# Optimization experiments

Hardware: AMD Instinct MI355X
Metric: run time of the kernel (lower is better)

## Reference

```python
import jax, jax.numpy as jnp
import numpy as np

B, T, D = 2, 2048, 1024
H = 16
HD = D // H  # 64


def setup_inputs() -> dict:
    key = jax.random.key(0)
    k1, k2, k3, k4, k5 = jax.random.split(key, 5)
    s = 0.02
    return {
        "x": jax.random.normal(k1, (B, T, D), dtype=jnp.float32),
        "Wqkv": jax.random.normal(k2, (D, 3 * D), dtype=jnp.float32) * s,
        "bqkv": jax.random.normal(k3, (3 * D,), dtype=jnp.float32) * s,
        "Wout": jax.random.normal(k4, (D, D), dtype=jnp.float32) * s,
        "bout": jax.random.normal(k5, (D,), dtype=jnp.float32) * s,
    }


def reference(x, Wqkv, bqkv, Wout, bout):
    b, t, c = x.shape
    qkv = (x @ Wqkv + bqkv).reshape(b, t, 3, H, HD)
    q = jnp.transpose(qkv[:, :, 0], (0, 2, 1, 3))  # [B,H,T,HD]
    k = jnp.transpose(qkv[:, :, 1], (0, 2, 1, 3))
    v = jnp.transpose(qkv[:, :, 2], (0, 2, 1, 3))
    att = jnp.einsum("bhqd,bhkd->bhqk", q, k) * (HD ** -0.5)
    mask = jnp.tril(jnp.ones((t, t), dtype=bool))  # causal, no past kv
    att = jnp.where(mask, att, -jnp.inf)
    att = jax.nn.softmax(att, axis=-1)
    y = jnp.einsum("bhqk,bhkd->bhqd", att, v)
    y = jnp.transpose(y, (0, 2, 1, 3)).reshape(b, t, c)
    return y @ Wout + bout
```

## Files before the change

kernel.cpp:

```cpp
#include <hip/hip_runtime.h>
#include <hip/hip_bf16.h>
#include <math.h>

#define B_  2
#define T_  2048
#define D_  1024
#define H_  16
#define HD_ 64

typedef __attribute__((ext_vector_type(8))) short short8;
typedef __attribute__((ext_vector_type(4))) float f32x4;

#if __has_builtin(__builtin_amdgcn_exp2f)
#define EXP2F __builtin_amdgcn_exp2f
#else
#define EXP2F exp2f
#endif

__device__ __forceinline__ ushort f2bf(float x) {
    unsigned u = __builtin_bit_cast(unsigned, x);
    return (ushort)((u + 0x7FFFu + ((u >> 16) & 1u)) >> 16);
}

__device__ __forceinline__ unsigned pack_bf2_fast(float a, float b) {
    unsigned ua = __builtin_bit_cast(unsigned, a) + 0x8000u;
    unsigned ub = __builtin_bit_cast(unsigned, b) + 0x8000u;
    return (ua >> 16) | (ub & 0xFFFF0000u);
}

__device__ __forceinline__ void load_lds_16B(const ushort* g, ushort* l) {
    __builtin_amdgcn_global_load_lds(
        (const __attribute__((address_space(1))) unsigned*)g,
        (__attribute__((address_space(3))) unsigned*)l, 16, 0, 0);
}

__global__ __launch_bounds__(256)
void prep_kernel(const float* __restrict__ x, ushort* __restrict__ xb,
                 const float* __restrict__ Wqkv, ushort* __restrict__ Wqkvt,
                 const float* __restrict__ Wout, ushort* __restrict__ Woutt)
{
    __shared__ ushort Ts[64][65];
    const int bid = blockIdx.x;

    if (bid < 512) {
        const int n4 = (B_ * T_ * D_) / 4;
        for (int i = bid * 256 + threadIdx.x; i < n4; i += 512 * 256) {
            float4 v = ((const float4*)x)[i];
            ushort4 o = { f2bf(v.x), f2bf(v.y), f2bf(v.z), f2bf(v.w) };
            ((ushort4*)xb)[i] = o;
        }
        return;
    }

    const float* W; ushort* Wt; int K, M, m0, k0;
    if (bid < 1280) {
        const int t = bid - 512;
        W = Wqkv; Wt = Wqkvt; K = D_; M = 3 * D_;
        m0 = (t % 48) * 64; k0 = (t / 48) * 64;
    } else {
        const int t = bid - 1280;
        W = Wout; Wt = Woutt; K = D_; M = D_;
        m0 = (t % 16) * 64; k0 = (t / 16) * 64;
    }

    const int tr = threadIdx.x >> 4;
    const int tc = threadIdx.x & 15;
    #pragma unroll
    for (int it = 0; it < 4; it++) {
        int k = tr + it * 16;
        float4 v = *(const float4*)&W[(size_t)(k0 + k) * M + m0 + tc * 4];
        Ts[tc * 4 + 0][k] = f2bf(v.x);
        Ts[tc * 4 + 1][k] = f2bf(v.y);
        Ts[tc * 4 + 2][k] = f2bf(v.z);
        Ts[tc * 4 + 3][k] = f2bf(v.w);
    }
    __syncthreads();
    #pragma unroll
    for (int it = 0; it < 2; it++) {
        const int mr  = (threadIdx.x >> 3) + it * 32;
        const int seg = (threadIdx.x & 7) * 8;
        short8 v;
        #pragma unroll
        for (int r = 0; r < 8; r++) v[r] = (short)Ts[mr][seg + r];
        *(short8*)&Wt[(size_t)(m0 + mr) * K + k0 + seg] = v;
    }
}

__global__ __launch_bounds__(256, 4)
void gemm_qkv(const ushort* __restrict__ A, const ushort* __restrict__ Bt,
              const float* __restrict__ bias,
              ushort* __restrict__ Qg, ushort* __restrict__ Kg,
              ushort* __restrict__ Vtg)
{
    const int K = D_;
    __shared__ __align__(16) ushort lds[16384];
    ushort* Asl = lds;
    ushort* Bsl = lds + 8192;

    const int tid = threadIdx.x;
    const int w  = tid >> 6, L = tid & 63;
    const int lt = L & 15, lq = L >> 4;
    const int wr = w >> 1, wc = w & 1;
    const int m0 = blockIdx.x * 128, n0 = blockIdx.y * 128;
    const int rsub = L >> 3;
    const int pgr  = L & 7;

    f32x4 acc[4][4] = {};

    for (int k0 = 0; k0 < K; k0 += 64) {
        __syncthreads();
        #pragma unroll
        for (int j = 0; j < 4; j++) {
            const int row  = (w * 4 + j) * 8 + rsub;
            const int gran = pgr ^ rsub;
            load_lds_16B(A  + (size_t)(n0 + row) * K + k0 + gran * 8,
                         &Asl[row * 64 + pgr * 8]);
            load_lds_16B(Bt + (size_t)(m0 + row) * K + k0 + gran * 8,
                         &Bsl[row * 64 + pgr * 8]);
        }
        __syncthreads();

        #pragma unroll
        for (int ks = 0; ks < 2; ks++) {
            short8 af[4], bf[4];
            #pragma unroll
            for (int i = 0; i < 4; i++) {
                const int ra = wr * 64 + i * 16 + lt;
                af[i] = *(const short8*)&Asl[ra * 64 + (((ks * 4 + lq) ^ (ra & 7)) * 8)];
                const int rb = wc * 64 + i * 16 + lt;
                bf[i] = *(const short8*)&Bsl[rb * 64 + (((ks * 4 + lq) ^ (rb & 7)) * 8)];
            }
            #pragma unroll
            for (int i = 0; i < 4; i++)
                #pragma unroll
                for (int j = 0; j < 4; j++)
                    acc[i][j] = __builtin_amdgcn_mfma_f32_16x16x32_bf16(af[i], bf[j], acc[i][j], 0, 0, 0);
        }
    }

    __syncthreads();
    const int s  = m0 >> 10;
    const int h0 = (m0 & 1023) >> 6;
    const float qs = (s == 0) ? 0.18033688011112042f : 1.0f;

    if (s < 2) {
        #pragma unroll
        for (int j = 0; j < 4; j++) {
            const int m  = wc * 64 + j * 16 + lt;
            const float bv = bias[m0 + m];
            #pragma unroll
            for (int i = 0; i < 4; i++) {
                const int n = wr * 64 + i * 16 + lq * 4;
                #pragma unroll
                for (int r = 0; r < 4; r++)
                    lds[(n + r) * 128 + m] = f2bf((acc[i][j][r] + bv) * qs);
            }
        }
        __syncthreads();
        ushort* dst = (s == 0 ? Qg : Kg);
        #pragma unroll
        for (int it = 0; it < 8; it++) {
            const int g   = tid + it * 256;
            const int row = g >> 4, c = g & 15;
            const int n = n0 + row;
            const int b = n >> 11, t = n & 2047;
            const int h = h0 + (c >> 3), d = (c & 7) * 8;
            short8 v = *(const short8*)&lds[row * 128 + c * 8];
            *(short8*)&dst[((size_t)(b * H_ + h) * T_ + t) * HD_ + d] = v;
        }
    } else {
        #pragma unroll
        for (int j = 0; j < 4; j++) {
            const int m  = wc * 64 + j * 16 + lt;
            const float bv = bias[m0 + m];
            #pragma unroll
            for (int i = 0; i < 4; i++) {
                const int n = wr * 64 + i * 16 + lq * 4;
                uint2 pk = { pack_bf2_fast(acc[i][j][0] + bv, acc[i][j][1] + bv),
                             pack_bf2_fast(acc[i][j][2] + bv, acc[i][j][3] + bv) };
                *(uint2*)&lds[m * 128 + n] = pk;
            }
        }
        __syncthreads();
        const int b = n0 >> 11, t0 = n0 & 2047;
        #pragma unroll
        for (int it = 0; it < 8; it++) {
            const int g   = tid + it * 256;
            const int row = g >> 4, c = g & 15;
            const int h = h0 + (row >> 6), d = row & 63;
            short8 v = *(const short8*)&lds[row * 128 + c * 8];
            *(short8*)&Vtg[((size_t)(b * H_ + h) * HD_ + d) * T_ + t0 + c * 8] = v;
        }
    }
}

__global__ __launch_bounds__(256, 4)
void gemm_out(const ushort* __restrict__ A, const ushort* __restrict__ Bt,
              const float* __restrict__ bias, float* __restrict__ C)
{
    const int K = D_, M = D_;
    __shared__ __align__(16) ushort lds[8192 + 4096];
    ushort* Asl = lds;
    ushort* Bsl = lds + 8192;

    const int tid = threadIdx.x;
    const int w  = tid >> 6, L = tid & 63;
    const int lt = L & 15, lq = L >> 4;
    const int wr = w >> 1, wc = w & 1;
    const int m0 = blockIdx.x * 64, n0 = blockIdx.y * 128;
    const int rsub = L >> 3;
    const int pgr  = L & 7;

    f32x4 acc[2][4] = {};

    for (int k0 = 0; k0 < K; k0 += 64) {
        __syncthreads();
        #pragma unroll
        for (int j = 0; j < 4; j++) {
            const int row  = (w * 4 + j) * 8 + rsub;
            const int gran = pgr ^ rsub;
            load_lds_16B(A + (size_t)(n0 + row) * K + k0 + gran * 8,
                         &Asl[row * 64 + pgr * 8]);
        }
        #pragma unroll
        for (int j = 0; j < 2; j++) {
            const int row  = (w * 2 + j) * 8 + rsub;
            const int gran = pgr ^ rsub;
            load_lds_16B(Bt + (size_t)(m0 + row) * K + k0 + gran * 8,
                         &Bsl[row * 64 + pgr * 8]);
        }
        __syncthreads();

        #pragma unroll
        for (int ks = 0; ks < 2; ks++) {
            short8 wf[2], yf[4];
            #pragma unroll
            for (int j = 0; j < 2; j++) {
                const int rb = wc * 32 + j * 16 + lt;
                wf[j] = *(const short8*)&Bsl[rb * 64 + (((ks * 4 + lq) ^ (rb & 7)) * 8)];
            }
            #pragma unroll
            for (int i = 0; i < 4; i++) {
                const int ra = wr * 64 + i * 16 + lt;
                yf[i] = *(const short8*)&Asl[ra * 64 + (((ks * 4 + lq) ^ (ra & 7)) * 8)];
            }
            #pragma unroll
            for (int j = 0; j < 2; j++)
                #pragma unroll
                for (int i = 0; i < 4; i++)
                    acc[j][i] = __builtin_amdgcn_mfma_f32_16x16x32_bf16(wf[j], yf[i], acc[j][i], 0, 0, 0);
        }
    }

    #pragma unroll
    for (int j = 0; j < 2; j++) {
        const int mbase = m0 + wc * 32 + j * 16 + lq * 4;
        const float4 bv = *(const float4*)&bias[mbase];
        #pragma unroll
        for (int i = 0; i < 4; i++) {
            const int n = n0 + wr * 64 + i * 16 + lt;
            float4 o = { acc[j][i][0] + bv.x, acc[j][i][1] + bv.y,
                         acc[j][i][2] + bv.z, acc[j][i][3] + bv.w };
            *(float4*)&C[(size_t)n * M + mbase] = o;
        }
    }
}

__global__ __launch_bounds__(256, 4)
void attn_mfma(const ushort* __restrict__ Qg, const ushort* __restrict__ Kg,
               const ushort* __restrict__ Vtg, ushort* __restrict__ yb)
{
    const int h = blockIdx.y, b = blockIdx.z;
    const int flip = ((blockIdx.y >> 3) ^ blockIdx.z) & 1;
    const int qb = flip ? blockIdx.x : (31 - blockIdx.x);
    const int tid = threadIdx.x;
    const int w  = tid >> 6, L = tid & 63;
    const int lt = L & 15, lq = L >> 4;

    __shared__ __align__(16) ushort Ks[128 * 64];
    __shared__ __align__(16) ushort Ps[4][640];

    const size_t bh = (size_t)(b * H_ + h);
    const ushort* Qbase  = Qg  + bh * T_ * HD_;
    const ushort* Kbase  = Kg  + bh * T_ * HD_;
    const ushort* Vf     = Vtg + bh * HD_ * T_ + (size_t)lt * T_ + lq * 8;

    const int q_glob = qb * 64 + w * 16 + lt;
    const short8 qf0 = *(const short8*)(Qbase + (size_t)q_glob * HD_ + lq * 8);
    const short8 qf1 = *(const short8*)(Qbase + (size_t)q_glob * HD_ + 32 + lq * 8);

    f32x4 acc_o[4] = {};
    float lsum = 0.f;

    const int krow = tid >> 3, kpg = tid & 7;
    const int nk = (qb + 2) >> 1;

    for (int kb = 0; kb < nk; kb++) {
        __syncthreads();
        #pragma unroll
        for (int rr = 0; rr < 4; rr++) {
            const int row = krow + 32 * rr;
            load_lds_16B(Kbase + (size_t)(kb * 128 + row) * HD_ + (kpg ^ (row & 7)) * 8,
                         &Ks[row * 64 + kpg * 8]);
        }
        __syncthreads();

        const bool last = (kb == nk - 1);
        const int ksN = (!last || (qb & 1)) ? 4 : 2;
        const int mk0 = last ? ((qb & 1) ? 2 : 0) : 4;

        for (int ks = 0; ks < ksN; ks++) {
            const int key0 = kb * 128 + ks * 32;
            const ushort* vp = Vf + key0;
            short8 vf0 = *(const short8*)(vp);
            short8 vf1 = *(const short8*)(vp + 16 * T_);
            short8 vf2 = *(const short8*)(vp + 32 * T_);
            short8 vf3 = *(const short8*)(vp + 48 * T_);

            const int row0 = (2 * ks) * 16 + lt;
            const int row1 = row0 + 16;
            short8 a00 = *(const short8*)&Ks[row0 * 64 + ((lq ^ (row0 & 7)) * 8)];
            short8 a01 = *(const short8*)&Ks[row0 * 64 + (((4 + lq) ^ (row0 & 7)) * 8)];
            short8 a10 = *(const short8*)&Ks[row1 * 64 + ((lq ^ (row1 & 7)) * 8)];
            short8 a11 = *(const short8*)&Ks[row1 * 64 + (((4 + lq) ^ (row1 & 7)) * 8)];
            f32x4 c0 = {}, c1 = {};
            c0 = __builtin_amdgcn_mfma_f32_16x16x32_bf16(a00, qf0, c0, 0, 0, 0);
            c0 = __builtin_amdgcn_mfma_f32_16x16x32_bf16(a01, qf1, c0, 0, 0, 0);
            c1 = __builtin_amdgcn_mfma_f32_16x16x32_bf16(a10, qf0, c1, 0, 0, 0);
            c1 = __builtin_amdgcn_mfma_f32_16x16x32_bf16(a11, qf1, c1, 0, 0, 0);

            float p[8];
            #pragma unroll
            for (int r = 0; r < 4; r++) { p[r] = EXP2F(c0[r]); p[4 + r] = EXP2F(c1[r]); }
            if (ks >= mk0) {
                const int kq = key0 + lq * 4;
                #pragma unroll
                for (int r = 0; r < 4; r++) {
                    if (kq + r > q_glob)      p[r] = 0.f;
                    if (kq + 16 + r > q_glob) p[4 + r] = 0.f;
                }
            }
            lsum += ((p[0] + p[1]) + (p[2] + p[3])) + ((p[4] + p[5]) + (p[6] + p[7]));
            *(uint2*)&Ps[w][lt * 40 + lq * 4] =
                (uint2){ pack_bf2_fast(p[0], p[1]), pack_bf2_fast(p[2], p[3]) };
            *(uint2*)&Ps[w][lt * 40 + 16 + lq * 4] =
                (uint2){ pack_bf2_fast(p[4], p[5]), pack_bf2_fast(p[6], p[7]) };

            short8 pf = *(const short8*)&Ps[w][lt * 40 + lq * 8];

            acc_o[0] = __builtin_amdgcn_mfma_f32_16x16x32_bf16(pf, vf0, acc_o[0], 0, 0, 0);
            acc_o[1] = __builtin_amdgcn_mfma_f32_16x16x32_bf16(pf, vf1, acc_o[1], 0, 0, 0);
            acc_o[2] = __builtin_amdgcn_mfma_f32_16x16x32_bf16(pf, vf2, acc_o[2], 0, 0, 0);
            acc_o[3] = __builtin_amdgcn_mfma_f32_16x16x32_bf16(pf, vf3, acc_o[3], 0, 0, 0);
        }
    }

    lsum += __shfl_xor(lsum, 16, 64);
    lsum += __shfl_xor(lsum, 32, 64);
    const float inv = 1.0f / lsum;

    float linv[4];
    #pragma unroll
    for (int r = 0; r < 4; r++) linv[r] = __shfl(inv, lq * 4 + r, 64);

    ushort* ybase = yb + (size_t)(b * T_ + qb * 64 + w * 16) * D_ + h * HD_;
    #pragma unroll
    for (int r = 0; r < 4; r++)
        #pragma unroll
        for (int dt = 0; dt < 4; dt++)
            ybase[(size_t)(lq * 4 + r) * D_ + dt * 16 + lt] = f2bf(acc_o[dt][r] * linv[r]);
}

extern "C" void kernel_launch(void* const* d_in, const int* in_sizes, int n_in,
                              void* d_out, int out_size, void* d_ws, size_t ws_size,
                              hipStream_t stream)
{
    const float* x    = (const float*)d_in[0];
    const float* Wqkv = (const float*)d_in[1];
    const float* bqkv = (const float*)d_in[2];
    const float* Wout = (const float*)d_in[3];
    const float* bout = (const float*)d_in[4];
    float* out = (float*)d_out;

    char* ws = (char*)d_ws;
    const size_t NT = (size_t)B_ * T_;
    ushort* xb     = (ushort*)ws;
    ushort* Wqkvt  = (ushort*)(ws + NT * D_ * 2);
    ushort* Woutt  = (ushort*)(ws + NT * D_ * 2 + (size_t)3 * D_ * D_ * 2);
    char*   p      = ws + NT * D_ * 2 + (size_t)4 * D_ * D_ * 2;
    const size_t qkv_elems = (size_t)B_ * H_ * T_ * HD_;
    ushort* Qg  = (ushort*)p;
    ushort* Kg  = (ushort*)(p + qkv_elems * 2);
    ushort* Vtg = (ushort*)(p + qkv_elems * 4);
    ushort* yb  = (ushort*)(p + qkv_elems * 6);

    prep_kernel<<<1536, 256, 0, stream>>>(x, xb, Wqkv, Wqkvt, Wout, Woutt);

    gemm_qkv<<<dim3(3 * D_ / 128, NT / 128), 256, 0, stream>>>(
        xb, Wqkvt, bqkv, Qg, Kg, Vtg);

    attn_mfma<<<dim3(32, H_, B_), 256, 0, stream>>>(Qg, Kg, Vtg, yb);

    gemm_out<<<dim3(D_ / 64, NT / 128), 256, 0, stream>>>(
        yb, Woutt, bout, out);
}
```

Baseline: 197.9 us.

## Double-buffer K and V tiles in LDS with 64-key blocks and fp16 PV

The attention kernel now stages both K and transposed V into double-buffered LDS tiles of 64 keys, prefetching the next tile while computing on the current one. Before, K was loaded in 128-key tiles between two barriers and V was read directly from global memory. Causal masking is now handled per diagonal block using each warp's index. V and P are now stored as fp16 rather than bf16, and the PV product uses the f16 MFMA, which gives extra mantissa precision at the cost of a narrower range. The aim is to hide global-load latency and cut uncoalesced V reads, in exchange for more LDS per block, which could lower occupancy.

```diff
diff --git a/kernel.cpp b/kernel.cpp
--- a/kernel.cpp
+++ b/kernel.cpp
@@ -9,6 +9,7 @@
 #define HD_ 64
 
 typedef __attribute__((ext_vector_type(8))) short short8;
+typedef __attribute__((ext_vector_type(8))) _Float16 half8;
 typedef __attribute__((ext_vector_type(4))) float f32x4;
 
 #if __has_builtin(__builtin_amdgcn_exp2f)
@@ -26,6 +27,10 @@
     unsigned ua = __builtin_bit_cast(unsigned, a) + 0x8000u;
     unsigned ub = __builtin_bit_cast(unsigned, b) + 0x8000u;
     return (ua >> 16) | (ub & 0xFFFF0000u);
+}
+
+__device__ __forceinline__ unsigned pack_h2(float a, float b) {
+    return __builtin_bit_cast(unsigned, __builtin_amdgcn_cvt_pkrtz(a, b));
 }
 
 __device__ __forceinline__ void load_lds_16B(const ushort* g, ushort* l) {
@@ -176,8 +181,8 @@
             #pragma unroll
             for (int i = 0; i < 4; i++) {
                 const int n = wr * 64 + i * 16 + lq * 4;
-                uint2 pk = { pack_bf2_fast(acc[i][j][0] + bv, acc[i][j][1] + bv),
-                             pack_bf2_fast(acc[i][j][2] + bv, acc[i][j][3] + bv) };
+                uint2 pk = { pack_h2(acc[i][j][0] + bv, acc[i][j][1] + bv),
+                             pack_h2(acc[i][j][2] + bv, acc[i][j][3] + bv) };
                 *(uint2*)&lds[m * 128 + n] = pk;
             }
         }
@@ -276,53 +281,64 @@
     const int tid = threadIdx.x;
     const int w  = tid >> 6, L = tid & 63;
     const int lt = L & 15, lq = L >> 4;
-
-    __shared__ __align__(16) ushort Ks[128 * 64];
-    __shared__ __align__(16) ushort Ps[4][640];
+    const int kswz = lt & 7;
+
+    __shared__ __align__(16) ushort Ks [2][64 * 64];
+    __shared__ __align__(16) ushort Vts[2][64 * 64];
+    __shared__ __align__(16) ushort Ps [4][640];
 
     const size_t bh = (size_t)(b * H_ + h);
     const ushort* Qbase  = Qg  + bh * T_ * HD_;
     const ushort* Kbase  = Kg  + bh * T_ * HD_;
-    const ushort* Vf     = Vtg + bh * HD_ * T_ + (size_t)lt * T_ + lq * 8;
-
-    const int q_glob = qb * 64 + w * 16 + lt;
+    const ushort* Vtbase = Vtg + bh * HD_ * T_;
+
+    const int q_in   = w * 16 + lt;
+    const int q_glob = qb * 64 + q_in;
     const short8 qf0 = *(const short8*)(Qbase + (size_t)q_glob * HD_ + lq * 8);
     const short8 qf1 = *(const short8*)(Qbase + (size_t)q_glob * HD_ + 32 + lq * 8);
 
     f32x4 acc_o[4] = {};
     float lsum = 0.f;
 
-    const int krow = tid >> 3, kpg = tid & 7;
-    const int nk = (qb + 2) >> 1;
+    const int srow = tid >> 3, spg = tid & 7;
+    const int nk = qb + 1;
+
+    #pragma unroll
+    for (int rr = 0; rr < 2; rr++) {
+        const int r = srow + 32 * rr;
+        load_lds_16B(Kbase + (size_t)r * HD_ + ((spg ^ (r & 7)) * 8),
+                     &Ks[0][r * 64 + spg * 8]);
+        load_lds_16B(Vtbase + (size_t)r * T_ + ((spg ^ (r & 7)) * 8),
+                     &Vts[0][r * 64 + spg * 8]);
+    }
 
     for (int kb = 0; kb < nk; kb++) {
-        __syncthreads();
-        #pragma unroll
-        for (int rr = 0; rr < 4; rr++) {
-            const int row = krow + 32 * rr;
-            load_lds_16B(Kbase + (size_t)(kb * 128 + row) * HD_ + (kpg ^ (row & 7)) * 8,
-                         &Ks[row * 64 + kpg * 8]);
-        }
-        __syncthreads();
-
-        const bool last = (kb == nk - 1);
-        const int ksN = (!last || (qb & 1)) ? 4 : 2;
-        const int mk0 = last ? ((qb & 1) ? 2 : 0) : 4;
+        const int cur = kb & 1;
+        __syncthreads();
+
+        if (kb + 1 < nk) {
+            const int nxt = cur ^ 1;
+            #pragma unroll
+            for (int rr = 0; rr < 2; rr++) {
+                const int r = srow + 32 * rr;
+                load_lds_16B(Kbase + (size_t)((kb + 1) * 64 + r) * HD_ + ((spg ^ (r & 7)) * 8),
+                             &Ks[nxt][r * 64 + spg * 8]);
+                load_lds_16B(Vtbase + (size_t)r * T_ + (kb + 1) * 64 + ((spg ^ (r & 7)) * 8),
+                             &Vts[nxt][r * 64 + spg * 8]);
+            }
+        }
+
+        const bool diag = (kb == nk - 1);
+        const int ksN = diag ? ((w >> 1) + 1) : 2;
+        const int mkc = diag ? (w >> 1) : 2;
 
         for (int ks = 0; ks < ksN; ks++) {
-            const int key0 = kb * 128 + ks * 32;
-            const ushort* vp = Vf + key0;
-            short8 vf0 = *(const short8*)(vp);
-            short8 vf1 = *(const short8*)(vp + 16 * T_);
-            short8 vf2 = *(const short8*)(vp + 32 * T_);
-            short8 vf3 = *(const short8*)(vp + 48 * T_);
-
-            const int row0 = (2 * ks) * 16 + lt;
+            const int row0 = ks * 32 + lt;
             const int row1 = row0 + 16;
-            short8 a00 = *(const short8*)&Ks[row0 * 64 + ((lq ^ (row0 & 7)) * 8)];
-            short8 a01 = *(const short8*)&Ks[row0 * 64 + (((4 + lq) ^ (row0 & 7)) * 8)];
-            short8 a10 = *(const short8*)&Ks[row1 * 64 + ((lq ^ (row1 & 7)) * 8)];
-            short8 a11 = *(const short8*)&Ks[row1 * 64 + (((4 + lq) ^ (row1 & 7)) * 8)];
+            short8 a00 = *(const short8*)&Ks[cur][row0 * 64 + ((lq ^ kswz) * 8)];
+            short8 a01 = *(const short8*)&Ks[cur][row0 * 64 + (((4 + lq) ^ kswz) * 8)];
+            short8 a10 = *(const short8*)&Ks[cur][row1 * 64 + ((lq ^ kswz) * 8)];
+            short8 a11 = *(const short8*)&Ks[cur][row1 * 64 + (((4 + lq) ^ kswz) * 8)];
             f32x4 c0 = {}, c1 = {};
             c0 = __builtin_amdgcn_mfma_f32_16x16x32_bf16(a00, qf0, c0, 0, 0, 0);
             c0 = __builtin_amdgcn_mfma_f32_16x16x32_bf16(a01, qf1, c0, 0, 0, 0);
@@ -332,26 +348,30 @@
             float p[8];
             #pragma unroll
             for (int r = 0; r < 4; r++) { p[r] = EXP2F(c0[r]); p[4 + r] = EXP2F(c1[r]); }
-            if (ks >= mk0) {
-                const int kq = key0 + lq * 4;
+            if (ks == mkc) {
+                const int key0 = ks * 32 + lq * 4;
                 #pragma unroll
                 for (int r = 0; r < 4; r++) {
-                    if (kq + r > q_glob)      p[r] = 0.f;
-                    if (kq + 16 + r > q_glob) p[4 + r] = 0.f;
+                    if (key0 + r > q_in)      p[r] = 0.f;
+                    if (key0 + 16 + r > q_in) p[4 + r] = 0.f;
                 }
             }
             lsum += ((p[0] + p[1]) + (p[2] + p[3])) + ((p[4] + p[5]) + (p[6] + p[7]));
             *(uint2*)&Ps[w][lt * 40 + lq * 4] =
-                (uint2){ pack_bf2_fast(p[0], p[1]), pack_bf2_fast(p[2], p[3]) };
+                (uint2){ pack_h2(p[0], p[1]), pack_h2(p[2], p[3]) };
             *(uint2*)&Ps[w][lt * 40 + 16 + lq * 4] =
-                (uint2){ pack_bf2_fast(p[4], p[5]), pack_bf2_fast(p[6], p[7]) };
-
-            short8 pf = *(const short8*)&Ps[w][lt * 40 + lq * 8];
-
-            acc_o[0] = __builtin_amdgcn_mfma_f32_16x16x32_bf16(pf, vf0, acc_o[0], 0, 0, 0);
-            acc_o[1] = __builtin_amdgcn_mfma_f32_16x16x32_bf16(pf, vf1, acc_o[1], 0, 0, 0);
-            acc_o[2] = __builtin_amdgcn_mfma_f32_16x16x32_bf16(pf, vf2, acc_o[2], 0, 0, 0);
-            acc_o[3] = __builtin_amdgcn_mfma_f32_16x16x32_bf16(pf, vf3, acc_o[3], 0, 0, 0);
+                (uint2){ pack_h2(p[4], p[5]), pack_h2(p[6], p[7]) };
+
+            half8 pf = __builtin_bit_cast(half8,
+                *(const short8*)&Ps[w][lt * 40 + lq * 8]);
+
+            #pragma unroll
+            for (int dt = 0; dt < 4; dt++) {
+                const int vr = dt * 16 + lt;
+                half8 vf = __builtin_bit_cast(half8,
+                    *(const short8*)&Vts[cur][vr * 64 + (((ks * 4 + lq) ^ kswz) * 8)]);
+                acc_o[dt] = __builtin_amdgcn_mfma_f32_16x16x32_f16(pf, vf, acc_o[dt], 0, 0, 0);
+            }
         }
     }
 
```

Result: faster. 172.1 us (-13.0%).
